# Kernel optimization log

Measured on AMD Instinct MI355X. Metric: run time of the kernel, lower is better.

## Reference

```python
import jax, jax.numpy as jnp
import numpy as np


def setup_inputs() -> dict:
    key = jax.random.key(0)
    nX, time_steps, T = 1024, 256, 10
    u0 = jax.random.normal(key, (nX, nX), dtype=jnp.float32)
    # learnable scalar diffusivity; 2e-4 keeps gamma <= 0.25 (stable scheme)
    alpha = jnp.asarray(2e-4, dtype=jnp.float32)
    return {"u0": u0, "alpha": alpha, "T": T, "nX": nX, "time_steps": time_steps}


def reference(u0, alpha, T, nX, time_steps):
    delta_x = 6.0 / (nX - 1)
    delta_t = T / (time_steps - 1)
    gamma = alpha * delta_t / delta_x ** 2

    # Torch code writes u0 at t=0, then zeroes all four boundaries for every t.
    u_init = jnp.zeros_like(u0).at[1:-1, 1:-1].set(u0[1:-1, 1:-1])

    def step(u, _):
        # 5-point Laplacian stencil on the interior; boundaries stay 0
        lap = (u[2:, 1:-1] + u[:-2, 1:-1] + u[1:-1, 2:] + u[1:-1, :-2]
               - 4.0 * u[1:-1, 1:-1])
        un = jnp.zeros_like(u).at[1:-1, 1:-1].set(gamma * lap + u[1:-1, 1:-1])
        return un, un

    _, us = jax.lax.scan(step, u_init, None, length=time_steps - 1)
    # u: [time_steps, nX, nX]
    return jnp.concatenate([u_init[None], us], axis=0)
```

## Files before the change

kernel.cpp:

```cpp
#include <hip/hip_runtime.h>
#include <math.h>


#define CORE 64
#define HALO 16
#define REG  96
#define PAD  100
#define TPB  1024
#define NIT  (94 * 24)

__device__ __forceinline__ void slot_init(int it, int o_r, int o_c, int nX,
                                          int& a, size_t& so, bool& st, float4& m) {
    const int r = 1 + it / 24;
    const int q = it % 24;
    a = r * PAD + 4 * q;
    const int gr  = o_r + r;
    const int gc0 = o_c + 4 * q;
    so = (size_t)gr * nX + gc0;
    st = (r >= HALO && r < HALO + CORE && q >= HALO / 4 && q < (REG - HALO) / 4);
    const bool rin = (gr > 0 && gr < nX - 1);
    m.x = (rin && gc0     > 0 && gc0     < nX - 1) ? 1.f : 0.f;
    m.y = (rin && gc0 + 1 > 0 && gc0 + 1 < nX - 1) ? 1.f : 0.f;
    m.z = (rin && gc0 + 2 > 0 && gc0 + 2 < nX - 1) ? 1.f : 0.f;
    m.w = (rin && gc0 + 3 > 0 && gc0 + 3 < nX - 1) ? 1.f : 0.f;
}

__device__ __forceinline__ void step_one(const float* __restrict__ bc,
                                         float* __restrict__ bn,
                                         float* __restrict__ of,
                                         int a, size_t so, bool st,
                                         const float4& m, float4& c, float gamma) {
    const float4 u4 = *reinterpret_cast<const float4*>(bc + a - PAD);
    const float4 d4 = *reinterpret_cast<const float4*>(bc + a + PAD);
    const float lf = bc[a - 1];
    const float rt = bc[a + 4];
    float4 o;
    o.x = m.x * (c.x + gamma * (u4.x + d4.x + lf  + c.y - 4.f * c.x));
    o.y = m.y * (c.y + gamma * (u4.y + d4.y + c.x + c.z - 4.f * c.y));
    o.z = m.z * (c.z + gamma * (u4.z + d4.z + c.y + c.w - 4.f * c.z));
    o.w = m.w * (c.w + gamma * (u4.w + d4.w + c.z + rt  - 4.f * c.w));
    *reinterpret_cast<float4*>(bn + a) = o;
    if (st) *reinterpret_cast<float4*>(of + so) = o;
    c = o;
}

__global__ __launch_bounds__(TPB)
void heat_fused(const float* __restrict__ src,
                float* __restrict__ out,
                int t_base, int k, int nX, int first,
                int time_steps,
                const float* __restrict__ alpha_p,
                const int* __restrict__ T_p) {
    __shared__ float buf[2][REG * PAD];

    const int tid = threadIdx.x;
    const int gb  = nX / CORE;
    const int bx  = blockIdx.x % gb;
    const int by  = blockIdx.x / gb;
    const int o_r = by * CORE - HALO;
    const int o_c = bx * CORE - HALO;

    const float alpha = *alpha_p;
    const float Tf    = (float)(*T_p);
    const float dx    = 6.0f / (float)(nX - 1);
    const float dt    = Tf / (float)(time_steps - 1);
    const float gamma = alpha * dt / (dx * dx);

    for (int idx = tid; idx < REG * PAD; idx += TPB) {
        const int r = idx / PAD, c = idx % PAD;
        const int gr = o_r + r, gc = o_c + c;
        float v = 0.f;
        if (c < REG && gr > 0 && gr < nX - 1 && gc > 0 && gc < nX - 1)
            v = src[(size_t)gr * nX + gc];
        buf[0][idx] = v;
        if (first && r >= HALO && r < HALO + CORE && c >= HALO && c < HALO + CORE)
            out[(size_t)gr * nX + gc] = v;
    }
    asm volatile("s_waitcnt lgkmcnt(0)" ::: "memory");
    __builtin_amdgcn_s_barrier();
    __builtin_amdgcn_sched_barrier(0);

    int a0, a1, a2 = PAD; size_t so0, so1, so2 = 0; bool st0, st1, st2 = false;
    float4 m0, m1, m2;
    slot_init(tid,           o_r, o_c, nX, a0, so0, st0, m0);
    slot_init(tid + TPB,     o_r, o_c, nX, a1, so1, st1, m1);
    const bool has2 = (tid + 2 * TPB) < NIT;
    if (has2) slot_init(tid + 2 * TPB, o_r, o_c, nX, a2, so2, st2, m2);

    float4 c0 = *reinterpret_cast<const float4*>(&buf[0][a0]);
    float4 c1 = *reinterpret_cast<const float4*>(&buf[0][a1]);
    float4 c2 = make_float4(0.f, 0.f, 0.f, 0.f);
    if (has2) c2 = *reinterpret_cast<const float4*>(&buf[0][a2]);

    int cur = 0;
    for (int s = 0; s < k; ++s) {
        const float* __restrict__ bc = buf[cur];
        float*       __restrict__ bn = buf[cur ^ 1];
        float* of = out + (size_t)(t_base + s + 1) * nX * nX;

        step_one(bc, bn, of, a0, so0, st0, m0, c0, gamma);
        step_one(bc, bn, of, a1, so1, st1, m1, c1, gamma);
        if (has2) step_one(bc, bn, of, a2, so2, st2, m2, c2, gamma);

        asm volatile("s_waitcnt lgkmcnt(0)" ::: "memory");
        __builtin_amdgcn_s_barrier();
        __builtin_amdgcn_sched_barrier(0);
        cur ^= 1;
    }
}

extern "C" void kernel_launch(void* const* d_in, const int* in_sizes, int n_in,
                              void* d_out, int out_size, void* d_ws, size_t ws_size,
                              hipStream_t stream) {
    const float* u0      = (const float*)d_in[0];
    const float* alpha_p = (const float*)d_in[1];
    const int*   T_p     = (const int*)d_in[2];

    const int n0 = in_sizes[0];
    const int nX = (int)(sqrtf((float)n0) + 0.5f);
    const int ts = out_size / n0;

    float* out = (float*)d_out;
    const int gb = nX / CORE;
    const int nblocks = gb * gb;

    for (int t = 0; t < ts - 1; t += HALO) {
        const int k = min(HALO, ts - 1 - t);
        const float* src = (t == 0) ? u0 : out + (size_t)t * n0;
        heat_fused<<<nblocks, TPB, 0, stream>>>(src, out, t, k, nX,
                                                (t == 0) ? 1 : 0, ts,
                                                alpha_p, T_p);
    }
}
```

Before: 343.2 us.

## Dedicate four warps to global stores, overlapping output writes with stencil compute

Splits the 1024-thread block into 768 compute threads and 256 writer threads. The compute threads advance the stencil in shared memory, while the writer threads copy the previous step's core tile from the shared buffer to global output behind the same barrier. This takes global store latency off the compute threads' critical path. In exchange, fewer threads share the stencil work, and the writer threads read a buffer that is written only on the step after next, which relies on the double-buffer timing.

```diff
diff --git a/kernel.cpp b/kernel.cpp
--- a/kernel.cpp
+++ b/kernel.cpp
@@ -7,17 +7,17 @@
 #define REG  96
 #define PAD  100
 #define TPB  1024
-#define NIT  (94 * 24)
+#define NCT  768
+#define NQ   24
+#define NIT  (94 * NQ)
 
 __device__ __forceinline__ void slot_init(int it, int o_r, int o_c, int nX,
-                                          int& a, size_t& so, bool& st, float4& m) {
-    const int r = 1 + it / 24;
-    const int q = it % 24;
+                                          int& a, float4& m) {
+    const int r = 1 + it / NQ;
+    const int q = it % NQ;
     a = r * PAD + 4 * q;
     const int gr  = o_r + r;
     const int gc0 = o_c + 4 * q;
-    so = (size_t)gr * nX + gc0;
-    st = (r >= HALO && r < HALO + CORE && q >= HALO / 4 && q < (REG - HALO) / 4);
     const bool rin = (gr > 0 && gr < nX - 1);
     m.x = (rin && gc0     > 0 && gc0     < nX - 1) ? 1.f : 0.f;
     m.y = (rin && gc0 + 1 > 0 && gc0 + 1 < nX - 1) ? 1.f : 0.f;
@@ -27,9 +27,8 @@
 
 __device__ __forceinline__ void step_one(const float* __restrict__ bc,
                                          float* __restrict__ bn,
-                                         float* __restrict__ of,
-                                         int a, size_t so, bool st,
-                                         const float4& m, float4& c, float gamma) {
+                                         int a, const float4& m, float4& c,
+                                         float gamma) {
     const float4 u4 = *reinterpret_cast<const float4*>(bc + a - PAD);
     const float4 d4 = *reinterpret_cast<const float4*>(bc + a + PAD);
     const float lf = bc[a - 1];
@@ -40,9 +39,14 @@
     o.z = m.z * (c.z + gamma * (u4.z + d4.z + c.y + c.w - 4.f * c.z));
     o.w = m.w * (c.w + gamma * (u4.w + d4.w + c.z + rt  - 4.f * c.w));
     *reinterpret_cast<float4*>(bn + a) = o;
-    if (st) *reinterpret_cast<float4*>(of + so) = o;
     c = o;
 }
+
+#define BAR() do { \
+    asm volatile("s_waitcnt lgkmcnt(0)" ::: "memory"); \
+    __builtin_amdgcn_s_barrier(); \
+    __builtin_amdgcn_sched_barrier(0); \
+} while (0)
 
 __global__ __launch_bounds__(TPB)
 void heat_fused(const float* __restrict__ src,
@@ -59,6 +63,7 @@
     const int by  = blockIdx.x / gb;
     const int o_r = by * CORE - HALO;
     const int o_c = bx * CORE - HALO;
+    const size_t n0 = (size_t)nX * nX;
 
     const float alpha = *alpha_p;
     const float Tf    = (float)(*T_p);
@@ -76,36 +81,57 @@
         if (first && r >= HALO && r < HALO + CORE && c >= HALO && c < HALO + CORE)
             out[(size_t)gr * nX + gc] = v;
     }
-    asm volatile("s_waitcnt lgkmcnt(0)" ::: "memory");
-    __builtin_amdgcn_s_barrier();
-    __builtin_amdgcn_sched_barrier(0);
+    BAR();
 
-    int a0, a1, a2 = PAD; size_t so0, so1, so2 = 0; bool st0, st1, st2 = false;
-    float4 m0, m1, m2;
-    slot_init(tid,           o_r, o_c, nX, a0, so0, st0, m0);
-    slot_init(tid + TPB,     o_r, o_c, nX, a1, so1, st1, m1);
-    const bool has2 = (tid + 2 * TPB) < NIT;
-    if (has2) slot_init(tid + 2 * TPB, o_r, o_c, nX, a2, so2, st2, m2);
+    if (tid < NCT) {
+        int a0, a1, a2 = PAD;
+        float4 m0, m1, m2 = make_float4(0.f, 0.f, 0.f, 0.f);
+        slot_init(tid,       o_r, o_c, nX, a0, m0);
+        slot_init(tid + NCT, o_r, o_c, nX, a1, m1);
+        const bool has2 = (tid + 2 * NCT) < NIT;
+        if (has2) slot_init(tid + 2 * NCT, o_r, o_c, nX, a2, m2);
 
-    float4 c0 = *reinterpret_cast<const float4*>(&buf[0][a0]);
-    float4 c1 = *reinterpret_cast<const float4*>(&buf[0][a1]);
-    float4 c2 = make_float4(0.f, 0.f, 0.f, 0.f);
-    if (has2) c2 = *reinterpret_cast<const float4*>(&buf[0][a2]);
+        float4 c0 = *reinterpret_cast<const float4*>(&buf[0][a0]);
+        float4 c1 = *reinterpret_cast<const float4*>(&buf[0][a1]);
+        float4 c2 = make_float4(0.f, 0.f, 0.f, 0.f);
+        if (has2) c2 = *reinterpret_cast<const float4*>(&buf[0][a2]);
 
-    int cur = 0;
-    for (int s = 0; s < k; ++s) {
-        const float* __restrict__ bc = buf[cur];
-        float*       __restrict__ bn = buf[cur ^ 1];
-        float* of = out + (size_t)(t_base + s + 1) * nX * nX;
-
-        step_one(bc, bn, of, a0, so0, st0, m0, c0, gamma);
-        step_one(bc, bn, of, a1, so1, st1, m1, c1, gamma);
-        if (has2) step_one(bc, bn, of, a2, so2, st2, m2, c2, gamma);
-
-        asm volatile("s_waitcnt lgkmcnt(0)" ::: "memory");
-        __builtin_amdgcn_s_barrier();
-        __builtin_amdgcn_sched_barrier(0);
-        cur ^= 1;
+        for (int s = 0; s < k; ++s) {
+            const float* __restrict__ bc = buf[s & 1];
+            float*       __restrict__ bn = buf[(s & 1) ^ 1];
+            step_one(bc, bn, a0, m0, c0, gamma);
+            step_one(bc, bn, a1, m1, c1, gamma);
+            if (has2) step_one(bc, bn, a2, m2, c2, gamma);
+            BAR();
+        }
+    } else {
+        const int wid = tid - NCT;
+        int wa[4]; size_t wo[4];
+        #pragma unroll
+        for (int j = 0; j < 4; ++j) {
+            const int idx = wid + 256 * j;
+            const int r = HALO + (idx >> 4);
+            const int q = (HALO / 4) + (idx & 15);
+            wa[j] = r * PAD + 4 * q;
+            wo[j] = (size_t)(o_r + r) * nX + (o_c + 4 * q);
+        }
+        for (int s = 0; s < k; ++s) {
+            if (s >= 1) {
+                const float* __restrict__ b = buf[s & 1];
+                float* of = out + (size_t)(t_base + s) * n0;
+                #pragma unroll
+                for (int j = 0; j < 4; ++j)
+                    *reinterpret_cast<float4*>(of + wo[j]) =
+                        *reinterpret_cast<const float4*>(b + wa[j]);
+            }
+            BAR();
+        }
+        const float* __restrict__ b = buf[k & 1];
+        float* of = out + (size_t)(t_base + k) * n0;
+        #pragma unroll
+        for (int j = 0; j < 4; ++j)
+            *reinterpret_cast<float4*>(of + wo[j]) =
+                *reinterpret_cast<const float4*>(b + wa[j]);
     }
 }
 
```

Measured after the change: 352.9 us. 2.8% more time.
